# Kernel tuning notes

Hardware: AMD Instinct MI355X
Metric: run time of the kernel (lower is better)

The kernel has to match this reference:

```python
import jax, jax.numpy as jnp
import numpy as np

NUM_HEADS = 8
LN_EPS = 1e-5


def setup_inputs() -> dict:
    key = jax.random.key(0)
    ks = jax.random.split(key, 9)
    B, C, H, W = 8, 512, 32, 32
    s = 1.0 / np.sqrt(C)
    return {
        "f_curr": jax.random.normal(ks[0], (B, C, H, W), dtype=jnp.float32),
        "f_prev": jax.random.normal(ks[1], (B, C, H, W), dtype=jnp.float32),
        "f_next": jax.random.normal(ks[2], (B, C, H, W), dtype=jnp.float32),
        "Wq": jax.random.normal(ks[3], (C, C), dtype=jnp.float32) * s,
        "Wk": jax.random.normal(ks[4], (C, C), dtype=jnp.float32) * s,
        "Wv": jax.random.normal(ks[5], (C, C), dtype=jnp.float32) * s,
        "Wo": jax.random.normal(ks[6], (C, C), dtype=jnp.float32) * s,
        "gamma": jnp.ones((C,), dtype=jnp.float32),
        "beta": jnp.zeros((C,), dtype=jnp.float32),
    }


def _flatten(f):
    # [B,C,H,W] -> [B, H*W, C]
    B, C, H, W = f.shape
    return f.reshape(B, C, H * W).transpose(0, 2, 1)


def reference(f_curr, f_prev, f_next, Wq, Wk, Wv, Wo, gamma, beta):
    B, C, H, W = f_curr.shape
    N = H * W
    hd = C // NUM_HEADS
    scale = hd ** -0.5

    curr_flat = _flatten(f_curr)                              # [B,N,C]
    neigh_flat = jnp.concatenate([_flatten(f_prev), _flatten(f_next)], axis=1)  # [B,2N,C]

    # torch Linear (no bias): y = x @ W.T
    Q = curr_flat @ Wq.T                                      # [B,N,C]
    K = neigh_flat @ Wk.T                                     # [B,2N,C]
    V = neigh_flat @ Wv.T                                     # [B,2N,C]

    def split_heads(t, L):
        return t.reshape(B, L, NUM_HEADS, hd).transpose(0, 2, 1, 3)  # [B,h,L,hd]

    Qh = split_heads(Q, N)
    Kh = split_heads(K, 2 * N)
    Vh = split_heads(V, 2 * N)

    scores = jnp.einsum("bhnd,bhmd->bhnm", Qh, Kh) * scale    # [B,h,N,2N]
    attn = jax.nn.softmax(scores, axis=-1)
    out = jnp.einsum("bhnm,bhmd->bhnd", attn, Vh)             # [B,h,N,hd]

    out = out.transpose(0, 2, 1, 3).reshape(B, N, C)          # merge heads
    out = curr_flat + out @ Wo.T                              # residual

    # LayerNorm over channel dim
    mu = jnp.mean(out, axis=-1, keepdims=True)
    var = jnp.mean(jnp.square(out - mu), axis=-1, keepdims=True)
    out = (out - mu) * jax.lax.rsqrt(var + LN_EPS) * gamma + beta

    return out.transpose(0, 2, 1).reshape(B, C, H, W)
```

## Files before the change

### kernel.cpp

```cpp
#include <hip/hip_runtime.h>
#include <hip/hip_bf16.h>
#include <math.h>

#define NH 8
#define HD 64
#define CH 512
#define NT 1024
#define NB 8

typedef __bf16 bf16_t;
typedef bf16_t bf16x8 __attribute__((ext_vector_type(8)));
typedef bf16_t bf16x4 __attribute__((ext_vector_type(4)));
typedef float  f32x4  __attribute__((ext_vector_type(4)));
typedef float  f32x16 __attribute__((ext_vector_type(16)));

#define MFMA16(a, b, c) __builtin_amdgcn_mfma_f32_16x16x32_bf16((a), (b), (c), 0, 0, 0)
#define MFMA32(a, b, c) __builtin_amdgcn_mfma_f32_32x32x16_bf16((a), (b), (c), 0, 0, 0)

__device__ __forceinline__ void gload16(const void* g, void* l) {
    __builtin_amdgcn_global_load_lds(
        (const __attribute__((address_space(1))) void*)g,
        (__attribute__((address_space(3))) void*)l, 16, 0, 0);
}

__global__ __launch_bounds__(256) void prep_kernel(
    const float* __restrict__ fc, const float* __restrict__ fp,
    const float* __restrict__ fn, bf16_t* __restrict__ Xc,
    bf16_t* __restrict__ Xn)
{
    __shared__ __align__(16) bf16_t tile[64 * 64];
    const int t = threadIdx.x;
    const int y = blockIdx.y;
    const int b = y / 3, ft = y % 3;
    const int c0 = (blockIdx.x & 7) * 64;
    const int n0 = (blockIdx.x >> 3) * 64;

    const float* src; bf16_t* dst;
    if (ft == 0)      { src = fc + (size_t)b * CH * NT; dst = Xc + (size_t)b * NT * CH; }
    else if (ft == 1) { src = fp + (size_t)b * CH * NT; dst = Xn + (size_t)b * 2 * NT * CH; }
    else              { src = fn + (size_t)b * CH * NT; dst = Xn + (size_t)b * 2 * NT * CH + (size_t)NT * CH; }

    const int nb = t & 15, cb = t >> 4;
    float4 ld[4];
#pragma unroll
    for (int i = 0; i < 4; ++i)
        ld[i] = *(const float4*)(src + (size_t)(c0 + cb * 4 + i) * NT + n0 + nb * 4);
    const float* lf = (const float*)ld;
#pragma unroll
    for (int j = 0; j < 4; ++j) {
        int n = nb * 4 + j;
        int v = (n >> 2) & 14;
        bf16x4 wv = { (bf16_t)lf[0 * 4 + j], (bf16_t)lf[1 * 4 + j],
                      (bf16_t)lf[2 * 4 + j], (bf16_t)lf[3 * 4 + j] };
        *(bf16x4*)(tile + n * 64 + ((cb ^ v) * 4)) = wv;
    }
    __syncthreads();
#pragma unroll
    for (int i = 0; i < 2; ++i) {
        int gid = t + i * 256;
        int n = gid >> 3, c16 = gid & 7;
        int v = (n >> 2) & 14;
        bf16x8 val = *(const bf16x8*)(tile + n * 64 + (((2 * c16) ^ v) * 4));
        *(bf16x8*)(dst + (size_t)(n0 + n) * CH + c0 + c16 * 8) = val;
    }
}

__global__ __launch_bounds__(256) void wcvt_kernel(
    const float* __restrict__ Wq, const float* __restrict__ Wk,
    const float* __restrict__ Wv, const float* __restrict__ Wo,
    bf16_t* __restrict__ Wb)
{
    const int m = blockIdx.y;
    const float* src = (m == 0) ? Wq : (m == 1) ? Wk : (m == 2) ? Wv : Wo;
    bf16_t* dst = Wb + (size_t)m * CH * CH;
    int gid = blockIdx.x * 256 + threadIdx.x;
    float4 v = *(const float4*)(src + (size_t)gid * 4);
    bf16x4 o = { (bf16_t)v.x, (bf16_t)v.y, (bf16_t)v.z, (bf16_t)v.w };
    *(bf16x4*)(dst + (size_t)gid * 4) = o;
}

template <bool SWAP>
__device__ __forceinline__ void gemm_core(const bf16_t* __restrict__ A,
                                          const bf16_t* __restrict__ B,
                                          bf16_t* aT, bf16_t* bT,
                                          f32x4 acc[4][4])
{
    const int t = threadIdx.x, w = t >> 6, lane = t & 63;
    const int lid = lane & 15, quad = lane >> 4;
    const int wm = w >> 1, wn = w & 1;
    const int l4 = lane >> 2, k4 = lane & 3;

    for (int kt = 0; kt < 16; ++kt) {
        const int k0 = kt * 32;
        __syncthreads();
#pragma unroll
        for (int i = 0; i < 2; ++i) {
            int q = w * 2 + i;
            int row = q * 16 + l4;
            int kk = k4 ^ ((row >> 1) & 3);
            gload16(A + (size_t)row * CH + k0 + kk * 8, aT + q * 512);
            gload16(B + (size_t)row * CH + k0 + kk * 8, bT + q * 512);
        }
        __syncthreads();

        const bf16_t* mT = SWAP ? bT : aT;
        const bf16_t* nT = SWAP ? aT : bT;
        bf16x8 mf[4], nf[4];
#pragma unroll
        for (int i = 0; i < 4; ++i) {
            int row = wm * 64 + i * 16 + lid;
            int kw = quad ^ ((row >> 1) & 3);
            mf[i] = *(const bf16x8*)(mT + row * 32 + kw * 8);
        }
#pragma unroll
        for (int i = 0; i < 4; ++i) {
            int row = wn * 64 + i * 16 + lid;
            int kw = quad ^ ((row >> 1) & 3);
            nf[i] = *(const bf16x8*)(nT + row * 32 + kw * 8);
        }
#pragma unroll
        for (int mi = 0; mi < 4; ++mi)
#pragma unroll
            for (int ni = 0; ni < 4; ++ni)
                acc[mi][ni] = MFMA16(mf[mi], nf[ni], acc[mi][ni]);
    }
}

__global__ __launch_bounds__(256) void qkv_kernel(
    const bf16_t* __restrict__ Xc, const bf16_t* __restrict__ Xn,
    const bf16_t* __restrict__ Wb,
    bf16_t* __restrict__ Qn, bf16_t* __restrict__ Kn, bf16_t* __restrict__ Vt)
{
    __shared__ __align__(16) bf16_t aT[128 * 32];
    __shared__ __align__(16) bf16_t bT[128 * 32];
    const int bx = blockIdx.x, b = blockIdx.y;
    const int t = threadIdx.x, w = t >> 6, lane = t & 63;
    const int lid = lane & 15, quad = lane >> 4;
    const int wm = w >> 1, wn = w & 1;
    const float QSC = 0.125f * 1.44269504f;

    f32x4 acc[4][4] = {};

    if (bx < 96) {
        const bf16_t* A; const bf16_t* B; bf16_t* O; float scale;
        if (bx < 32) {
            int nt = bx >> 2, ct = bx & 3;
            A = Xc + (size_t)b * NT * CH + (size_t)nt * 128 * CH;
            B = Wb + (size_t)0 * CH * CH + (size_t)ct * 128 * CH;
            O = Qn + (size_t)b * NT * CH + (size_t)nt * 128 * CH + ct * 128;
            scale = QSC;
        } else {
            int j = bx - 32, nt = j >> 2, ct = j & 3;
            A = Xn + (size_t)b * 2 * NT * CH + (size_t)nt * 128 * CH;
            B = Wb + (size_t)1 * CH * CH + (size_t)ct * 128 * CH;
            O = Kn + (size_t)b * 2 * NT * CH + (size_t)nt * 128 * CH + ct * 128;
            scale = 1.0f;
        }
        gemm_core<false>(A, B, aT, bT, acc);
#pragma unroll
        for (int mi = 0; mi < 4; ++mi)
#pragma unroll
            for (int ni = 0; ni < 4; ++ni)
#pragma unroll
                for (int r = 0; r < 4; ++r) {
                    int n  = wm * 64 + mi * 16 + quad * 4 + r;
                    int co = wn * 64 + ni * 16 + lid;
                    O[(size_t)n * CH + co] = (bf16_t)(acc[mi][ni][r] * scale);
                }
    } else {
        int j = bx - 96, nt = j >> 2, ct = j & 3;
        const bf16_t* A = Xn + (size_t)b * 2 * NT * CH + (size_t)nt * 128 * CH;
        const bf16_t* B = Wb + (size_t)2 * CH * CH + (size_t)ct * 128 * CH;
        bf16_t* O = Vt + (size_t)b * CH * 2 * NT + (size_t)ct * 128 * 2 * NT + nt * 128;
        gemm_core<true>(A, B, aT, bT, acc);
#pragma unroll
        for (int mi = 0; mi < 4; ++mi)
#pragma unroll
            for (int ni = 0; ni < 4; ++ni)
#pragma unroll
                for (int r = 0; r < 4; ++r) {
                    int co_l  = wm * 64 + mi * 16 + quad * 4 + r;
                    int key_l = wn * 64 + ni * 16 + lid;
                    O[(size_t)co_l * (2 * NT) + key_l] = (bf16_t)acc[mi][ni][r];
                }
    }
}

__global__ __launch_bounds__(256) void attn_kernel(
    const bf16_t* __restrict__ Qn, const bf16_t* __restrict__ Kn,
    const bf16_t* __restrict__ Vt, bf16_t* __restrict__ AOn)
{
    __shared__ __align__(16) bf16_t kv[128 * 72];
    __shared__ __align__(16) float  pqf[9216];
    __shared__ float l_scr[128];

    bf16_t* pq = (bf16_t*)pqf;

    const int t = threadIdx.x;
    const int w = t >> 6, lane = t & 63;
    const int wq = w >> 1, wk = w & 1;
    const int l31 = lane & 31, h = lane >> 5;

    const int q0 = blockIdx.x * 128;
    const int hh = blockIdx.y, b = blockIdx.z;

    const bf16_t* Qb  = Qn + ((size_t)b * NT + q0) * CH + hh * HD;
    const bf16_t* Kb  = Kn + (size_t)b * 2 * NT * CH + hh * HD;
    const bf16_t* Vtb = Vt + ((size_t)b * CH + hh * HD) * (2 * NT);
    bf16_t* AOb = AOn + ((size_t)b * NT + q0) * CH + hh * HD;

#pragma unroll
    for (int i = 0; i < 4; ++i) {
        int gid = t + i * 256;
        int qr = gid >> 3, c8 = (gid & 7) * 8;
        *(bf16x8*)(pq + qr * 72 + (c8 ^ (qr & 24))) =
            *(const bf16x8*)(Qb + (size_t)qr * CH + c8);
    }
    __syncthreads();

    bf16x8 kreg[4];
#pragma unroll
    for (int i = 0; i < 4; ++i) {
        int gid = t + i * 256;
        int kr = gid >> 3, c8 = (gid & 7) * 8;
        kreg[i] = *(const bf16x8*)(Kb + (size_t)kr * CH + c8);
    }

    bf16x8 qf[2][4];
#pragma unroll
    for (int nf = 0; nf < 2; ++nf)
#pragma unroll
        for (int ks = 0; ks < 4; ++ks) {
            int row = wq * 64 + nf * 32 + l31;
            int col = (ks * 16 + h * 8) ^ (row & 24);
            qf[nf][ks] = *(const bf16x8*)(pq + row * 72 + col);
        }
    __syncthreads();

    bf16_t* pw = pq + w * 4608;

    f32x16 o[2][2] = {};
    float lpart[2] = {0.f, 0.f};

    for (int kt = 0; kt < 16; ++kt) {
        const int kbase = kt * 128;

#pragma unroll
        for (int i = 0; i < 4; ++i) {
            int gid = t + i * 256;
            int kr = gid >> 3, c8 = (gid & 7) * 8;
            *(bf16x8*)(kv + kr * 72 + (c8 ^ (kr & 24))) = kreg[i];
        }
        __syncthreads();

        bf16x8 vreg[4];
#pragma unroll
        for (int i = 0; i < 4; ++i) {
            int gid = t + i * 256;
            int dr = gid >> 4, c8 = (gid & 15) * 8;
            vreg[i] = *(const bf16x8*)(Vtb + (size_t)dr * (2 * NT) + kbase + c8);
        }

        f32x16 s[2][2] = {};
#pragma unroll
        for (int ks = 0; ks < 4; ++ks) {
            bf16x8 af[2];
#pragma unroll
            for (int mf = 0; mf < 2; ++mf) {
                int arow = wk * 64 + mf * 32 + l31;
                int acol = (ks * 16 + h * 8) ^ (arow & 24);
                af[mf] = *(const bf16x8*)(kv + arow * 72 + acol);
            }
#pragma unroll
            for (int mf = 0; mf < 2; ++mf)
#pragma unroll
                for (int nf = 0; nf < 2; ++nf)
                    s[mf][nf] = MFMA32(af[mf], qf[nf][ks], s[mf][nf]);
        }

#pragma unroll
        for (int mf = 0; mf < 2; ++mf)
#pragma unroll
            for (int nf = 0; nf < 2; ++nf) {
                int qrow = nf * 32 + l31;
#pragma unroll
                for (int g = 0; g < 4; ++g) {
                    float p0 = exp2f(s[mf][nf][4 * g + 0]);
                    float p1 = exp2f(s[mf][nf][4 * g + 1]);
                    float p2 = exp2f(s[mf][nf][4 * g + 2]);
                    float p3 = exp2f(s[mf][nf][4 * g + 3]);
                    lpart[nf] += (p0 + p1) + (p2 + p3);
                    bf16x4 pk = { (bf16_t)p0, (bf16_t)p1, (bf16_t)p2, (bf16_t)p3 };
                    int kb = mf * 32 + 8 * g + 4 * h;
                    *(bf16x4*)(pw + qrow * 72 + (kb ^ (qrow & 24))) = pk;
                }
            }
        __syncthreads();

#pragma unroll
        for (int i = 0; i < 4; ++i) {
            int gid = t + i * 256;
            int dr = gid >> 4, c8 = (gid & 15) * 8;
            *(bf16x8*)(kv + dr * 136 + (c8 ^ (dr & 24))) = vreg[i];
        }
        __syncthreads();

        const int nb2 = (kt < 15) ? kbase + 128 : kbase;
#pragma unroll
        for (int i = 0; i < 4; ++i) {
            int gid = t + i * 256;
            int kr = gid >> 3, c8 = (gid & 7) * 8;
            kreg[i] = *(const bf16x8*)(Kb + (size_t)(nb2 + kr) * CH + c8);
        }

#pragma unroll
        for (int ks = 0; ks < 4; ++ks) {
            bf16x8 av[2], bp[2];
#pragma unroll
            for (int df = 0; df < 2; ++df) {
                int vrow = df * 32 + l31;
                int vcol = (wk * 64 + ks * 16 + h * 8) ^ (vrow & 24);
                av[df] = *(const bf16x8*)(kv + vrow * 136 + vcol);
            }
#pragma unroll
            for (int nf = 0; nf < 2; ++nf) {
                int bq = nf * 32 + l31;
                int bcol = (ks * 16 + h * 8) ^ (bq & 24);
                bp[nf] = *(const bf16x8*)(pw + bq * 72 + bcol);
            }
#pragma unroll
            for (int df = 0; df < 2; ++df)
#pragma unroll
                for (int nf = 0; nf < 2; ++nf)
                    o[df][nf] = MFMA32(av[df], bp[nf], o[df][nf]);
        }
        __syncthreads();
    }

    float l2[2];
#pragma unroll
    for (int nf = 0; nf < 2; ++nf)
        l2[nf] = lpart[nf] + __shfl_xor(lpart[nf], 32);

    if (wk == 1) {
        float* scr = pqf + wq * 4352;
#pragma unroll
        for (int df = 0; df < 2; ++df)
#pragma unroll
            for (int nf = 0; nf < 2; ++nf) {
                int qrow = nf * 32 + l31;
#pragma unroll
                for (int g = 0; g < 4; ++g) {
                    int d = df * 32 + 8 * g + 4 * h;
                    f32x4 v = { o[df][nf][4 * g + 0], o[df][nf][4 * g + 1],
                                o[df][nf][4 * g + 2], o[df][nf][4 * g + 3] };
                    *(f32x4*)(scr + qrow * 68 + d) = v;
                }
            }
        if (h == 0) {
            l_scr[wq * 64 + 0 * 32 + l31] = l2[0];
            l_scr[wq * 64 + 1 * 32 + l31] = l2[1];
        }
    }
    __syncthreads();

    if (wk == 0) {
        const float* scr = pqf + wq * 4352;
        float inv[2];
#pragma unroll
        for (int nf = 0; nf < 2; ++nf)
            inv[nf] = 1.0f / (l2[nf] + l_scr[wq * 64 + nf * 32 + l31]);
#pragma unroll
        for (int df = 0; df < 2; ++df)
#pragma unroll
            for (int nf = 0; nf < 2; ++nf) {
                int qrow = nf * 32 + l31;
#pragma unroll
                for (int g = 0; g < 4; ++g) {
                    int d = df * 32 + 8 * g + 4 * h;
                    f32x4 part = *(const f32x4*)(scr + qrow * 68 + d);
                    bf16x4 ov = {
                        (bf16_t)((o[df][nf][4 * g + 0] + part.x) * inv[nf]),
                        (bf16_t)((o[df][nf][4 * g + 1] + part.y) * inv[nf]),
                        (bf16_t)((o[df][nf][4 * g + 2] + part.z) * inv[nf]),
                        (bf16_t)((o[df][nf][4 * g + 3] + part.w) * inv[nf]) };
                    int qg = wq * 64 + qrow;
                    *(bf16x4*)(kv + qg * 72 + (d ^ (qg & 24))) = ov;
                }
            }
    }
    __syncthreads();

#pragma unroll
    for (int i = 0; i < 4; ++i) {
        int gid = t + i * 256;
        int qr = gid >> 3, c8 = (gid & 7) * 8;
        *(bf16x8*)(AOb + (size_t)qr * CH + c8) =
            *(const bf16x8*)(kv + qr * 72 + (c8 ^ (qr & 24)));
    }
}

__global__ __launch_bounds__(256) void proj_kernel(
    const bf16_t* __restrict__ AOn, const bf16_t* __restrict__ Wb,
    const float* __restrict__ fc, float* __restrict__ Zt)
{
    __shared__ __align__(16) bf16_t aT[128 * 32];
    __shared__ __align__(16) bf16_t bT[128 * 32];
    const int bx = blockIdx.x, b = blockIdx.y;
    const int nt = bx >> 2, ct = bx & 3;
    const int t = threadIdx.x, w = t >> 6, lane = t & 63;
    const int lid = lane & 15, quad = lane >> 4;
    const int wm = w >> 1, wn = w & 1;

    const bf16_t* A = AOn + (size_t)b * NT * CH + (size_t)nt * 128 * CH;
    const bf16_t* B = Wb + (size_t)3 * CH * CH + (size_t)ct * 128 * CH;

    f32x4 acc[4][4] = {};
    gemm_core<true>(A, B, aT, bT, acc);

    const size_t bofs = (size_t)b * CH * NT;
#pragma unroll
    for (int mi = 0; mi < 4; ++mi)
#pragma unroll
        for (int ni = 0; ni < 4; ++ni)
#pragma unroll
            for (int r = 0; r < 4; ++r) {
                int co_l = wm * 64 + mi * 16 + quad * 4 + r;
                int n_l  = wn * 64 + ni * 16 + lid;
                size_t idx = bofs + (size_t)(ct * 128 + co_l) * NT + nt * 128 + n_l;
                Zt[idx] = acc[mi][ni][r] + fc[idx];
            }
}

__global__ __launch_bounds__(256) void stats_kernel(
    const float* __restrict__ Zt, float* __restrict__ mu_buf,
    float* __restrict__ rs_buf)
{
    __shared__ float sS[1024], sQ[1024];
    const int b = blockIdx.y, n0 = blockIdx.x * 64;
    const int t = threadIdx.x, w = t >> 6, lane = t & 63;
    const int co_off = lane >> 4, n4 = lane & 15;
    const float* Zb = Zt + (size_t)b * CH * NT + n0 + n4 * 4;

    f32x4 s = {0, 0, 0, 0}, q = {0, 0, 0, 0};
    for (int it = 0; it < 32; ++it) {
        int co = w * 4 + co_off + it * 16;
        f32x4 z = *(const f32x4*)(Zb + (size_t)co * NT);
#pragma unroll
        for (int c = 0; c < 4; ++c) { s[c] += z[c]; q[c] += z[c] * z[c]; }
    }
#pragma unroll
    for (int c = 0; c < 4; ++c) { sS[t * 4 + c] = s[c]; sQ[t * 4 + c] = q[c]; }
    __syncthreads();

    if (t < 64) {
        int n4r = t >> 2, comp = t & 3;
        float ss = 0.f, qq = 0.f;
#pragma unroll
        for (int i = 0; i < 16; ++i) {
            int idx = ((i >> 2) * 64 + (i & 3) * 16 + n4r) * 4 + comp;
            ss += sS[idx]; qq += sQ[idx];
        }
        float mu  = ss * (1.0f / 512.0f);
        float var = qq * (1.0f / 512.0f) - mu * mu;
        mu_buf[(size_t)b * NT + n0 + t] = mu;
        rs_buf[(size_t)b * NT + n0 + t] = rsqrtf(var + 1e-5f);
    }
}

__global__ __launch_bounds__(256) void apply_kernel(
    const float* __restrict__ Zt, const float* __restrict__ mu_buf,
    const float* __restrict__ rs_buf, const float* __restrict__ gamma,
    const float* __restrict__ beta, float* __restrict__ out)
{
    const int row = blockIdx.x;
    const int co = row & 511, b = row >> 9;
    const int t = threadIdx.x;
    const float g = gamma[co], be = beta[co];
    const size_t base = (size_t)row * NT + t * 4;
    f32x4 z  = *(const f32x4*)(Zt + base);
    f32x4 mu = *(const f32x4*)(mu_buf + (size_t)b * NT + t * 4);
    f32x4 rs = *(const f32x4*)(rs_buf + (size_t)b * NT + t * 4);
    f32x4 o;
#pragma unroll
    for (int c = 0; c < 4; ++c) o[c] = (z[c] - mu[c]) * rs[c] * g + be;
    *(f32x4*)(out + base) = o;
}

extern "C" void kernel_launch(void* const* d_in, const int* in_sizes, int n_in,
                              void* d_out, int out_size, void* d_ws, size_t ws_size,
                              hipStream_t stream)
{
    (void)in_sizes; (void)n_in; (void)out_size; (void)ws_size;
    const float* fc    = (const float*)d_in[0];
    const float* fp    = (const float*)d_in[1];
    const float* fn    = (const float*)d_in[2];
    const float* Wq    = (const float*)d_in[3];
    const float* Wk    = (const float*)d_in[4];
    const float* Wv    = (const float*)d_in[5];
    const float* Wo    = (const float*)d_in[6];
    const float* gamma = (const float*)d_in[7];
    const float* beta  = (const float*)d_in[8];
    float* out = (float*)d_out;

    char* ws = (char*)d_ws;
    bf16_t* Xn  = (bf16_t*)(ws);
    bf16_t* Qn  = (bf16_t*)(ws + 16777216);
    bf16_t* Kn  = (bf16_t*)(ws + 25165824);
    bf16_t* Xc  = (bf16_t*)(ws + 41943040);
    bf16_t* AOn = Xc;
    bf16_t* Vt  = (bf16_t*)(ws + 50331648);
    bf16_t* Wb  = (bf16_t*)(ws + 67108864);
    float*  mu  = (float*)(ws + 69206016);
    float*  rs  = (float*)(ws + 69238784);
    float*  Zt  = (float*)(ws);

    prep_kernel<<<dim3(128, 24), 256, 0, stream>>>(fc, fp, fn, Xc, Xn);
    wcvt_kernel<<<dim3(256, 4), 256, 0, stream>>>(Wq, Wk, Wv, Wo, Wb);
    qkv_kernel<<<dim3(160, 8), 256, 0, stream>>>(Xc, Xn, Wb, Qn, Kn, Vt);
    attn_kernel<<<dim3(8, 8, 8), 256, 0, stream>>>(Qn, Kn, Vt, AOn);
    proj_kernel<<<dim3(32, 8), 256, 0, stream>>>(AOn, Wb, fc, Zt);
    stats_kernel<<<dim3(16, 8), 256, 0, stream>>>(Zt, mu, rs);
    apply_kernel<<<4096, 256, 0, stream>>>(Zt, mu, rs, gamma, beta, out);
}
```

Measured before the change: 252.4 us.

## Double-buffer K/V in attention, keep P in registers via permlane swap

The attention kernel now double-buffers K and V tiles in LDS and prefetches the tile two steps ahead, which removes two barriers per iteration. The softmax probabilities are packed with v_cvt_pk_bf16_f32 and rearranged with v_permlane32_swap so they feed the PV MFMA straight from registers instead of going through LDS. It also adds s_setprio around the MFMA sections, remaps the 1D grid so blocks sharing a batch and head land on the same XCD for L2 reuse, and declares launch_bounds(256,2). In exchange it uses about 72KB of LDS and more registers, which may limit occupancy.

```diff
diff --git a/kernel.cpp b/kernel.cpp
--- a/kernel.cpp
+++ b/kernel.cpp
@@ -13,6 +13,7 @@
 typedef bf16_t bf16x4 __attribute__((ext_vector_type(4)));
 typedef float  f32x4  __attribute__((ext_vector_type(4)));
 typedef float  f32x16 __attribute__((ext_vector_type(16)));
+typedef unsigned u32x4 __attribute__((ext_vector_type(4)));
 
 #define MFMA16(a, b, c) __builtin_amdgcn_mfma_f32_16x16x32_bf16((a), (b), (c), 0, 0, 0)
 #define MFMA32(a, b, c) __builtin_amdgcn_mfma_f32_32x32x16_bf16((a), (b), (c), 0, 0, 0)
@@ -21,6 +22,16 @@
     __builtin_amdgcn_global_load_lds(
         (const __attribute__((address_space(1))) void*)g,
         (__attribute__((address_space(3))) void*)l, 16, 0, 0);
+}
+
+__device__ __forceinline__ unsigned cvtpk(float lo, float hi) {
+    unsigned r;
+    asm("v_cvt_pk_bf16_f32 %0, %1, %2" : "=v"(r) : "v"(lo), "v"(hi));
+    return r;
+}
+
+__device__ __forceinline__ void plswap(unsigned& a, unsigned& b) {
+    asm("v_permlane32_swap_b32 %0, %1" : "+v"(a), "+v"(b));
 }
 
 __global__ __launch_bounds__(256) void prep_kernel(
@@ -186,45 +197,59 @@
     }
 }
 
-__global__ __launch_bounds__(256) void attn_kernel(
+__global__ __launch_bounds__(256, 2) void attn_kernel(
     const bf16_t* __restrict__ Qn, const bf16_t* __restrict__ Kn,
     const bf16_t* __restrict__ Vt, bf16_t* __restrict__ AOn)
 {
-    __shared__ __align__(16) bf16_t kv[128 * 72];
-    __shared__ __align__(16) float  pqf[9216];
-    __shared__ float l_scr[128];
-
-    bf16_t* pq = (bf16_t*)pqf;
+    __shared__ __align__(16) char smem[72192];
+    bf16_t* const kbuf0 = (bf16_t*)smem;
+    bf16_t* const kbuf1 = (bf16_t*)(smem + 18432);
+    bf16_t* const vbuf0 = (bf16_t*)(smem + 36864);
+    bf16_t* const vbuf1 = (bf16_t*)(smem + 54272);
+    float*  const l_scr = (float*)(smem + 71680);
 
     const int t = threadIdx.x;
     const int w = t >> 6, lane = t & 63;
     const int wq = w >> 1, wk = w & 1;
     const int l31 = lane & 31, h = lane >> 5;
 
-    const int q0 = blockIdx.x * 128;
-    const int hh = blockIdx.y, b = blockIdx.z;
+    const int bid = blockIdx.x;
+    const int xcd = bid & 7, ii = bid >> 3;
+    const int grp = xcd * 8 + (ii >> 3);
+    const int qt  = ii & 7;
+    const int b = grp >> 3, hh = grp & 7;
+    const int q0 = qt * 128;
 
     const bf16_t* Qb  = Qn + ((size_t)b * NT + q0) * CH + hh * HD;
     const bf16_t* Kb  = Kn + (size_t)b * 2 * NT * CH + hh * HD;
     const bf16_t* Vtb = Vt + ((size_t)b * CH + hh * HD) * (2 * NT);
     bf16_t* AOb = AOn + ((size_t)b * NT + q0) * CH + hh * HD;
 
+    bf16x8 kreg[4], vreg[4];
 #pragma unroll
     for (int i = 0; i < 4; ++i) {
         int gid = t + i * 256;
         int qr = gid >> 3, c8 = (gid & 7) * 8;
-        *(bf16x8*)(pq + qr * 72 + (c8 ^ (qr & 24))) =
+        *(bf16x8*)(kbuf1 + qr * 72 + (c8 ^ (qr & 24))) =
             *(const bf16x8*)(Qb + (size_t)qr * CH + c8);
     }
-    __syncthreads();
-
-    bf16x8 kreg[4];
 #pragma unroll
     for (int i = 0; i < 4; ++i) {
         int gid = t + i * 256;
         int kr = gid >> 3, c8 = (gid & 7) * 8;
         kreg[i] = *(const bf16x8*)(Kb + (size_t)kr * CH + c8);
-    }
+        int dr = gid >> 4, c16 = (gid & 15) * 8;
+        vreg[i] = *(const bf16x8*)(Vtb + (size_t)dr * (2 * NT) + c16);
+    }
+#pragma unroll
+    for (int i = 0; i < 4; ++i) {
+        int gid = t + i * 256;
+        int kr = gid >> 3, c8 = (gid & 7) * 8;
+        *(bf16x8*)(kbuf0 + kr * 72 + (c8 ^ (kr & 24))) = kreg[i];
+        int dr = gid >> 4, c16 = (gid & 15) * 8;
+        *(bf16x8*)(vbuf0 + dr * 136 + (c16 ^ (dr & 24))) = vreg[i];
+    }
+    __syncthreads();
 
     bf16x8 qf[2][4];
 #pragma unroll
@@ -233,35 +258,50 @@
         for (int ks = 0; ks < 4; ++ks) {
             int row = wq * 64 + nf * 32 + l31;
             int col = (ks * 16 + h * 8) ^ (row & 24);
-            qf[nf][ks] = *(const bf16x8*)(pq + row * 72 + col);
-        }
+            qf[nf][ks] = *(const bf16x8*)(kbuf1 + row * 72 + col);
+        }
+#pragma unroll
+    for (int i = 0; i < 4; ++i) {
+        int gid = t + i * 256;
+        int kr = gid >> 3, c8 = (gid & 7) * 8;
+        kreg[i] = *(const bf16x8*)(Kb + (size_t)(128 + kr) * CH + c8);
+        int dr = gid >> 4, c16 = (gid & 15) * 8;
+        vreg[i] = *(const bf16x8*)(Vtb + (size_t)dr * (2 * NT) + 128 + c16);
+    }
     __syncthreads();
-
-    bf16_t* pw = pq + w * 4608;
 
     f32x16 o[2][2] = {};
     float lpart[2] = {0.f, 0.f};
 
     for (int kt = 0; kt < 16; ++kt) {
-        const int kbase = kt * 128;
+        const int cur = kt & 1;
+        bf16_t* const kb_w = cur ? kbuf0 : kbuf1;
+        bf16_t* const vb_w = cur ? vbuf0 : vbuf1;
+        const bf16_t* const kb_r = cur ? kbuf1 : kbuf0;
+        const bf16_t* const vb_r = cur ? vbuf1 : vbuf0;
 
 #pragma unroll
         for (int i = 0; i < 4; ++i) {
             int gid = t + i * 256;
             int kr = gid >> 3, c8 = (gid & 7) * 8;
-            *(bf16x8*)(kv + kr * 72 + (c8 ^ (kr & 24))) = kreg[i];
-        }
-        __syncthreads();
-
-        bf16x8 vreg[4];
-#pragma unroll
-        for (int i = 0; i < 4; ++i) {
-            int gid = t + i * 256;
-            int dr = gid >> 4, c8 = (gid & 15) * 8;
-            vreg[i] = *(const bf16x8*)(Vtb + (size_t)dr * (2 * NT) + kbase + c8);
+            *(bf16x8*)(kb_w + kr * 72 + (c8 ^ (kr & 24))) = kreg[i];
+            int dr = gid >> 4, c16 = (gid & 15) * 8;
+            *(bf16x8*)(vb_w + dr * 136 + (c16 ^ (dr & 24))) = vreg[i];
+        }
+        {
+            const int pfb = (kt + 2 < 16) ? (kt + 2) * 128 : 0;
+#pragma unroll
+            for (int i = 0; i < 4; ++i) {
+                int gid = t + i * 256;
+                int kr = gid >> 3, c8 = (gid & 7) * 8;
+                kreg[i] = *(const bf16x8*)(Kb + (size_t)(pfb + kr) * CH + c8);
+                int dr = gid >> 4, c16 = (gid & 15) * 8;
+                vreg[i] = *(const bf16x8*)(Vtb + (size_t)dr * (2 * NT) + pfb + c16);
+            }
         }
 
         f32x16 s[2][2] = {};
+        __builtin_amdgcn_s_setprio(1);
 #pragma unroll
         for (int ks = 0; ks < 4; ++ks) {
             bf16x8 af[2];
@@ -269,7 +309,7 @@
             for (int mf = 0; mf < 2; ++mf) {
                 int arow = wk * 64 + mf * 32 + l31;
                 int acol = (ks * 16 + h * 8) ^ (arow & 24);
-                af[mf] = *(const bf16x8*)(kv + arow * 72 + acol);
+                af[mf] = *(const bf16x8*)(kb_r + arow * 72 + acol);
             }
 #pragma unroll
             for (int mf = 0; mf < 2; ++mf)
@@ -277,62 +317,48 @@
                 for (int nf = 0; nf < 2; ++nf)
                     s[mf][nf] = MFMA32(af[mf], qf[nf][ks], s[mf][nf]);
         }
-
-#pragma unroll
-        for (int mf = 0; mf < 2; ++mf)
+        __builtin_amdgcn_s_setprio(0);
+
+#pragma unroll
+        for (int mf = 0; mf < 2; ++mf) {
+            bf16x8 pfrag[2][2];
 #pragma unroll
             for (int nf = 0; nf < 2; ++nf) {
-                int qrow = nf * 32 + l31;
-#pragma unroll
-                for (int g = 0; g < 4; ++g) {
-                    float p0 = exp2f(s[mf][nf][4 * g + 0]);
-                    float p1 = exp2f(s[mf][nf][4 * g + 1]);
-                    float p2 = exp2f(s[mf][nf][4 * g + 2]);
-                    float p3 = exp2f(s[mf][nf][4 * g + 3]);
-                    lpart[nf] += (p0 + p1) + (p2 + p3);
-                    bf16x4 pk = { (bf16_t)p0, (bf16_t)p1, (bf16_t)p2, (bf16_t)p3 };
-                    int kb = mf * 32 + 8 * g + 4 * h;
-                    *(bf16x4*)(pw + qrow * 72 + (kb ^ (qrow & 24))) = pk;
+                float p[16];
+#pragma unroll
+                for (int r = 0; r < 16; ++r) p[r] = exp2f(s[mf][nf][r]);
+                lpart[nf] += ((p[0] + p[1]) + (p[2] + p[3]))
+                           + ((p[4] + p[5]) + (p[6] + p[7]))
+                           + ((p[8] + p[9]) + (p[10] + p[11]))
+                           + ((p[12] + p[13]) + (p[14] + p[15]));
+                unsigned a0 = cvtpk(p[0], p[1]),   b0 = cvtpk(p[4], p[5]);
+                unsigned a1 = cvtpk(p[2], p[3]),   b1 = cvtpk(p[6], p[7]);
+                unsigned a2 = cvtpk(p[8], p[9]),   b2 = cvtpk(p[12], p[13]);
+                unsigned a3 = cvtpk(p[10], p[11]), b3 = cvtpk(p[14], p[15]);
+                plswap(a0, b0); plswap(a1, b1); plswap(a2, b2); plswap(a3, b3);
+                u32x4 f0 = { a0, a1, b0, b1 };
+                u32x4 f1 = { a2, a3, b2, b3 };
+                pfrag[nf][0] = __builtin_bit_cast(bf16x8, f0);
+                pfrag[nf][1] = __builtin_bit_cast(bf16x8, f1);
+            }
+            __builtin_amdgcn_s_setprio(1);
+#pragma unroll
+            for (int fi = 0; fi < 2; ++fi) {
+                const int ks = mf * 2 + fi;
+                bf16x8 av[2];
+#pragma unroll
+                for (int df = 0; df < 2; ++df) {
+                    int vrow = df * 32 + l31;
+                    int vcol = (wk * 64 + ks * 16 + h * 8) ^ (vrow & 24);
+                    av[df] = *(const bf16x8*)(vb_r + vrow * 136 + vcol);
                 }
-            }
-        __syncthreads();
-
-#pragma unroll
-        for (int i = 0; i < 4; ++i) {
-            int gid = t + i * 256;
-            int dr = gid >> 4, c8 = (gid & 15) * 8;
-            *(bf16x8*)(kv + dr * 136 + (c8 ^ (dr & 24))) = vreg[i];
-        }
-        __syncthreads();
-
-        const int nb2 = (kt < 15) ? kbase + 128 : kbase;
-#pragma unroll
-        for (int i = 0; i < 4; ++i) {
-            int gid = t + i * 256;
-            int kr = gid >> 3, c8 = (gid & 7) * 8;
-            kreg[i] = *(const bf16x8*)(Kb + (size_t)(nb2 + kr) * CH + c8);
-        }
-
-#pragma unroll
-        for (int ks = 0; ks < 4; ++ks) {
-            bf16x8 av[2], bp[2];
-#pragma unroll
-            for (int df = 0; df < 2; ++df) {
-                int vrow = df * 32 + l31;
-                int vcol = (wk * 64 + ks * 16 + h * 8) ^ (vrow & 24);
-                av[df] = *(const bf16x8*)(kv + vrow * 136 + vcol);
-            }
-#pragma unroll
-            for (int nf = 0; nf < 2; ++nf) {
-                int bq = nf * 32 + l31;
-                int bcol = (ks * 16 + h * 8) ^ (bq & 24);
-                bp[nf] = *(const bf16x8*)(pw + bq * 72 + bcol);
-            }
-#pragma unroll
-            for (int df = 0; df < 2; ++df)
-#pragma unroll
-                for (int nf = 0; nf < 2; ++nf)
-                    o[df][nf] = MFMA32(av[df], bp[nf], o[df][nf]);
+#pragma unroll
+                for (int df = 0; df < 2; ++df)
+#pragma unroll
+                    for (int nf = 0; nf < 2; ++nf)
+                        o[df][nf] = MFMA32(av[df], pfrag[nf][fi], o[df][nf]);
+            }
+            __builtin_amdgcn_s_setprio(0);
         }
         __syncthreads();
     }
@@ -342,8 +368,11 @@
     for (int nf = 0; nf < 2; ++nf)
         l2[nf] = lpart[nf] + __shfl_xor(lpart[nf], 32);
 
+    float* const scr_all = (float*)smem;
+    bf16_t* const obuf = (bf16_t*)(smem + 36864);
+
     if (wk == 1) {
-        float* scr = pqf + wq * 4352;
+        float* scr = scr_all + wq * 4352;
 #pragma unroll
         for (int df = 0; df < 2; ++df)
 #pragma unroll
@@ -365,7 +394,7 @@
     __syncthreads();
 
     if (wk == 0) {
-        const float* scr = pqf + wq * 4352;
+        const float* scr = scr_all + wq * 4352;
         float inv[2];
 #pragma unroll
         for (int nf = 0; nf < 2; ++nf)
@@ -385,7 +414,7 @@
                         (bf16_t)((o[df][nf][4 * g + 2] + part.z) * inv[nf]),
                         (bf16_t)((o[df][nf][4 * g + 3] + part.w) * inv[nf]) };
                     int qg = wq * 64 + qrow;
-                    *(bf16x4*)(kv + qg * 72 + (d ^ (qg & 24))) = ov;
+                    *(bf16x4*)(obuf + qg * 72 + (d ^ (qg & 24))) = ov;
                 }
             }
     }
@@ -396,7 +425,7 @@
         int gid = t + i * 256;
         int qr = gid >> 3, c8 = (gid & 7) * 8;
         *(bf16x8*)(AOb + (size_t)qr * CH + c8) =
-            *(const bf16x8*)(kv + qr * 72 + (c8 ^ (qr & 24)));
+            *(const bf16x8*)(obuf + qr * 72 + (c8 ^ (qr & 24)));
     }
 }
 
@@ -518,7 +547,7 @@
     prep_kernel<<<dim3(128, 24), 256, 0, stream>>>(fc, fp, fn, Xc, Xn);
     wcvt_kernel<<<dim3(256, 4), 256, 0, stream>>>(Wq, Wk, Wv, Wo, Wb);
     qkv_kernel<<<dim3(160, 8), 256, 0, stream>>>(Xc, Xn, Wb, Qn, Kn, Vt);
-    attn_kernel<<<dim3(8, 8, 8), 256, 0, stream>>>(Qn, Kn, Vt, AOn);
+    attn_kernel<<<dim3(512), 256, 0, stream>>>(Qn, Kn, Vt, AOn);
     proj_kernel<<<dim3(32, 8), 256, 0, stream>>>(AOn, Wb, fc, Zt);
     stats_kernel<<<dim3(16, 8), 256, 0, stream>>>(Zt, mu, rs);
     apply_kernel<<<4096, 256, 0, stream>>>(Zt, mu, rs, gamma, beta, out);
```

New measurement: 239.9 us. -4.9%, faster.
